# Kernel optimization log

Hardware: AMD Instinct MI355X
Metric: run time of the kernel (lower is better)

Reference implementation:

```python
import jax, jax.numpy as jnp
import numpy as np

IN_SIZE = 65536
HIDDEN = 128
D_STEPS = 64   # nd_actions[0]
N_ACT = 512    # nd_actions[1]


def setup_inputs() -> dict:
    key = jax.random.key(0)
    ks = jax.random.split(key, 7)
    s = 1.0 / np.sqrt(HIDDEN)  # torch LSTMCell/Linear init scale (uniform); use scaled normal
    return {
        "x": jax.random.normal(ks[0], (IN_SIZE,), jnp.float32),
        "w_ih": jax.random.normal(ks[1], (4 * HIDDEN, IN_SIZE), jnp.float32) * s,
        "w_hh": jax.random.normal(ks[2], (4 * HIDDEN, HIDDEN), jnp.float32) * s,
        "b_ih": jax.random.normal(ks[3], (4 * HIDDEN,), jnp.float32) * s,
        "b_hh": jax.random.normal(ks[4], (4 * HIDDEN,), jnp.float32) * s,
        "w_lin": jax.random.normal(ks[5], (N_ACT, HIDDEN), jnp.float32) * s,
        "b_lin": jax.random.normal(ks[6], (N_ACT,), jnp.float32) * s,
    }


def reference(x, w_ih, w_hh, b_ih, b_hh, w_lin, b_lin):
    # x is constant across the D steps, so its gate contribution is computed once.
    ihx = w_ih @ x + b_ih + b_hh  # (4H,)
    h0 = jnp.zeros((HIDDEN,), x.dtype)
    c0 = jnp.zeros((HIDDEN,), x.dtype)

    def step(carry, _):
        h, c = carry
        gates = ihx + w_hh @ h  # (4H,)
        i, f, g, o = jnp.split(gates, 4)  # torch LSTMCell gate order: i, f, g, o
        c = jax.nn.sigmoid(f) * c + jax.nn.sigmoid(i) * jnp.tanh(g)
        h = jax.nn.sigmoid(o) * jnp.tanh(c)
        logits = w_lin @ h + b_lin  # (N,)
        return (h, c), logits

    _, action_probs = jax.lax.scan(step, (h0, c0), None, length=D_STEPS)
    return action_probs  # (D, N)
```

## Files before the change

kernel.cpp:

```cpp
#include <hip/hip_runtime.h>
#include <hip/hip_bf16.h>

#define IN_SIZE 65536
#define HIDDEN 128
#define D_STEPS 64
#define N_ACT 512

typedef _Float16 half2_ __attribute__((ext_vector_type(2)));
typedef _Float16 half4_ __attribute__((ext_vector_type(4)));
typedef _Float16 half8_ __attribute__((ext_vector_type(8)));
typedef float f32x4 __attribute__((ext_vector_type(4)));

__device__ __forceinline__ float rcp_(float x) {
#if __has_builtin(__builtin_amdgcn_rcpf)
    return __builtin_amdgcn_rcpf(x);
#else
    return 1.f / x;
#endif
}
__device__ __forceinline__ float exp2_(float x) {
#if __has_builtin(__builtin_amdgcn_exp2f)
    return __builtin_amdgcn_exp2f(x);
#else
    return __exp2f(x);
#endif
}
#define L2E 1.44269504088896340736f

__global__ __launch_bounds__(256) void k_ihx(const float* __restrict__ w_ih,
                                             const float* __restrict__ x,
                                             float* __restrict__ partials) {
    int bid = blockIdx.x;
    int rp = bid >> 3;
    int ck = bid & 7;
    int t = threadIdx.x;
    int r0 = 2 * rp, r1 = 2 * rp + 1;
    const float4* xp = (const float4*)(x + ck * 8192);
    const float4* w0 = (const float4*)(w_ih + (size_t)r0 * IN_SIZE + ck * 8192);
    const float4* w1 = (const float4*)(w_ih + (size_t)r1 * IN_SIZE + ck * 8192);

    float4 xv[8];
#pragma unroll
    for (int i = 0; i < 8; ++i) xv[i] = xp[t + i * 256];

    float a0 = 0.f, a1 = 0.f;
#pragma unroll
    for (int i = 0; i < 8; ++i) {
        float4 w4 = w0[t + i * 256];
        a0 += w4.x * xv[i].x + w4.y * xv[i].y + w4.z * xv[i].z + w4.w * xv[i].w;
    }
#pragma unroll
    for (int i = 0; i < 8; ++i) {
        float4 w4 = w1[t + i * 256];
        a1 += w4.x * xv[i].x + w4.y * xv[i].y + w4.z * xv[i].z + w4.w * xv[i].w;
    }
#pragma unroll
    for (int off = 32; off; off >>= 1) {
        a0 += __shfl_down(a0, off, 64);
        a1 += __shfl_down(a1, off, 64);
    }
    __shared__ float s[8];
    if ((t & 63) == 0) { s[t >> 6] = a0; s[4 + (t >> 6)] = a1; }
    __syncthreads();
    if (t == 0) {
        partials[r0 * 8 + ck] = s[0] + s[1] + s[2] + s[3];
        partials[r1 * 8 + ck] = s[4] + s[5] + s[6] + s[7];
    }
}

__global__ __attribute__((amdgpu_flat_work_group_size(512, 512)))
__attribute__((amdgpu_waves_per_eu(2, 2)))
void k_rec_logits(
    const float* __restrict__ w_hh,
    const float* __restrict__ b_ih,
    const float* __restrict__ b_hh,
    const float* __restrict__ w_lin,
    const float* __restrict__ b_lin,
    const float* __restrict__ partials,
    float* __restrict__ out) {
    int t = threadIdx.x;
    int b = blockIdx.x;
    int w = t >> 6;
    int l = t & 63;
    int lg = l >> 4;
    int lm = l & 15;

    __shared__ _Float16 whh_s[4 * HIDDEN * HIDDEN];
    __shared__ half8_ h_v[2][16];
    __shared__ float h_keep[HIDDEN];
    __shared__ float ihx_s[4 * HIDDEN];

    {
        const float2* src = (const float2*)w_hh;
        half2_* dst = (half2_*)whh_s;
#pragma unroll 4
        for (int i = 0; i < 64; ++i) {
            float2 v = src[i * 512 + t];
            half2_ p = {(_Float16)v.x, (_Float16)v.y};
            dst[i * 512 + t] = p;
        }
    }
    {
        const float4* pp = (const float4*)(partials + t * 8);
        float4 p0 = pp[0], p1 = pp[1];
        ihx_s[t] = p0.x + p0.y + p0.z + p0.w + p1.x + p1.y + p1.z + p1.w +
                   b_ih[t] + b_hh[t];
    }
    if (t < 16) {
        half8_ z = {(_Float16)0.f, (_Float16)0.f, (_Float16)0.f, (_Float16)0.f,
                    (_Float16)0.f, (_Float16)0.f, (_Float16)0.f, (_Float16)0.f};
        h_v[0][t] = z;
    }
    __syncthreads();

    half8_ afrag[4][4];
#pragma unroll
    for (int G = 0; G < 4; ++G) {
#pragma unroll
        for (int kt = 0; kt < 4; ++kt) {
            afrag[G][kt] = *(const half8_*)&whh_s[(size_t)(G * HIDDEN + 16 * w + lm) * HIDDEN
                                                  + kt * 32 + lg * 8];
        }
    }
    f32x4 ihxv[4];
#pragma unroll
    for (int G = 0; G < 4; ++G)
        ihxv[G] = *(const f32x4*)&ihx_s[G * HIDDEN + 16 * w + lg * 4];

    asm volatile(""
        : "+v"(afrag[0][0]), "+v"(afrag[0][1]), "+v"(afrag[0][2]), "+v"(afrag[0][3]),
          "+v"(afrag[1][0]), "+v"(afrag[1][1]), "+v"(afrag[1][2]), "+v"(afrag[1][3]),
          "+v"(afrag[2][0]), "+v"(afrag[2][1]), "+v"(afrag[2][2]), "+v"(afrag[2][3]),
          "+v"(afrag[3][0]), "+v"(afrag[3][1]), "+v"(afrag[3][2]), "+v"(afrag[3][3]),
          "+v"(ihxv[0]), "+v"(ihxv[1]), "+v"(ihxv[2]), "+v"(ihxv[3]));

    int r2 = lm & 3;
    bool s1 = (r2 & 1) != 0, s2 = (r2 & 2) != 0;
    float c_own = 0.f;

    for (int d = 0; d < D_STEPS; ++d) {
        int rb = d & 1, wb = rb ^ 1;
        half8_ bf0 = h_v[rb][0 * 4 + lg];
        half8_ bf1 = h_v[rb][1 * 4 + lg];
        half8_ bf2 = h_v[rb][2 * 4 + lg];
        half8_ bf3 = h_v[rb][3 * 4 + lg];
        f32x4 ai_ = ihxv[0];
        f32x4 af_ = ihxv[1];
        f32x4 ag_ = ihxv[2];
        f32x4 ao_ = ihxv[3];
#define MFMA __builtin_amdgcn_mfma_f32_16x16x32_f16
        ai_ = MFMA(afrag[0][0], bf0, ai_, 0, 0, 0);
        af_ = MFMA(afrag[1][0], bf0, af_, 0, 0, 0);
        ag_ = MFMA(afrag[2][0], bf0, ag_, 0, 0, 0);
        ao_ = MFMA(afrag[3][0], bf0, ao_, 0, 0, 0);
        ai_ = MFMA(afrag[0][1], bf1, ai_, 0, 0, 0);
        af_ = MFMA(afrag[1][1], bf1, af_, 0, 0, 0);
        ag_ = MFMA(afrag[2][1], bf1, ag_, 0, 0, 0);
        ao_ = MFMA(afrag[3][1], bf1, ao_, 0, 0, 0);
        ai_ = MFMA(afrag[0][2], bf2, ai_, 0, 0, 0);
        af_ = MFMA(afrag[1][2], bf2, af_, 0, 0, 0);
        ag_ = MFMA(afrag[2][2], bf2, ag_, 0, 0, 0);
        ao_ = MFMA(afrag[3][2], bf2, ao_, 0, 0, 0);
        ai_ = MFMA(afrag[0][3], bf3, ai_, 0, 0, 0);
        af_ = MFMA(afrag[1][3], bf3, af_, 0, 0, 0);
        ag_ = MFMA(afrag[2][3], bf3, ag_, 0, 0, 0);
        ao_ = MFMA(afrag[3][3], bf3, ao_, 0, 0, 0);
#undef MFMA
        float gi = s2 ? (s1 ? ai_[3] : ai_[2]) : (s1 ? ai_[1] : ai_[0]);
        float gf = s2 ? (s1 ? af_[3] : af_[2]) : (s1 ? af_[1] : af_[0]);
        float gg = s2 ? (s1 ? ag_[3] : ag_[2]) : (s1 ? ag_[1] : ag_[0]);
        float go = s2 ? (s1 ? ao_[3] : ao_[2]) : (s1 ? ao_[1] : ao_[0]);
        float ig = rcp_(1.f + exp2_(-L2E * gi));
        float fg = rcp_(1.f + exp2_(-L2E * gf));
        float gt = 2.f * rcp_(1.f + exp2_(-2.f * L2E * gg)) - 1.f;
        float og = rcp_(1.f + exp2_(-L2E * go));
        c_own = fg * c_own + ig * gt;
        float th = 2.f * rcp_(1.f + exp2_(-2.f * L2E * c_own)) - 1.f;
        float h = og * th;
        if (lm < 4) {
            int cell = 16 * w + lg * 4 + r2;
            ((_Float16*)&h_v[wb][0])[cell] = (_Float16)h;
            if (d == b) h_keep[cell] = h;
        }
        __syncthreads();
    }

    {
        const float4* wl = (const float4*)(w_lin + (size_t)t * HIDDEN);
        float acc = b_lin[t];
#pragma unroll
        for (int k = 0; k < HIDDEN / 4; ++k) {
            float4 w4 = wl[k];
            acc += w4.x * h_keep[4 * k + 0] + w4.y * h_keep[4 * k + 1] +
                   w4.z * h_keep[4 * k + 2] + w4.w * h_keep[4 * k + 3];
        }
        out[b * N_ACT + t] = acc;
    }
}

extern "C" void kernel_launch(void* const* d_in, const int* in_sizes, int n_in,
                              void* d_out, int out_size, void* d_ws, size_t ws_size,
                              hipStream_t stream) {
    const float* x     = (const float*)d_in[0];
    const float* w_ih  = (const float*)d_in[1];
    const float* w_hh  = (const float*)d_in[2];
    const float* b_ih  = (const float*)d_in[3];
    const float* b_hh  = (const float*)d_in[4];
    const float* w_lin = (const float*)d_in[5];
    const float* b_lin = (const float*)d_in[6];
    float* out = (float*)d_out;

    float* partials = (float*)d_ws;

    k_ihx<<<2048, 256, 0, stream>>>(w_ih, x, partials);
    k_rec_logits<<<D_STEPS, 512, 0, stream>>>(w_hh, b_ih, b_hh, w_lin, b_lin,
                                              partials, out);
}
```

Baseline: 69.69 us.

## Halve recurrence block to 4 waves, each computing 32 hidden units

The recurrent kernel now runs 256 threads (4 waves) per block instead of 512. Each wave holds twice as many W_hh fragments in registers and issues 32 MFMAs per step covering 32 hidden cells. The intent is to make the per-step __syncthreads barrier cheaper with fewer waves, at the cost of longer MFMA chains per wave and higher register pressure. Setup and the final logits loop are split across two rows per thread to cover the same work.

```diff
diff --git a/kernel.cpp b/kernel.cpp
--- a/kernel.cpp
+++ b/kernel.cpp
@@ -7,7 +7,6 @@
 #define N_ACT 512
 
 typedef _Float16 half2_ __attribute__((ext_vector_type(2)));
-typedef _Float16 half4_ __attribute__((ext_vector_type(4)));
 typedef _Float16 half8_ __attribute__((ext_vector_type(8)));
 typedef float f32x4 __attribute__((ext_vector_type(4)));
 
@@ -68,8 +67,8 @@
     }
 }
 
-__global__ __attribute__((amdgpu_flat_work_group_size(512, 512)))
-__attribute__((amdgpu_waves_per_eu(2, 2)))
+__global__ __attribute__((amdgpu_flat_work_group_size(256, 256)))
+__attribute__((amdgpu_waves_per_eu(1, 1)))
 void k_rec_logits(
     const float* __restrict__ w_hh,
     const float* __restrict__ b_ih,
@@ -83,7 +82,7 @@
     int w = t >> 6;
     int l = t & 63;
     int lg = l >> 4;
-    int lm = l & 15;
+    int n  = l & 15;
 
     __shared__ _Float16 whh_s[4 * HIDDEN * HIDDEN];
     __shared__ half8_ h_v[2][16];
@@ -93,18 +92,20 @@
     {
         const float2* src = (const float2*)w_hh;
         half2_* dst = (half2_*)whh_s;
-#pragma unroll 4
-        for (int i = 0; i < 64; ++i) {
-            float2 v = src[i * 512 + t];
+#pragma unroll 8
+        for (int i = 0; i < 128; ++i) {
+            float2 v = src[i * 256 + t];
             half2_ p = {(_Float16)v.x, (_Float16)v.y};
-            dst[i * 512 + t] = p;
+            dst[i * 256 + t] = p;
         }
     }
-    {
-        const float4* pp = (const float4*)(partials + t * 8);
+#pragma unroll
+    for (int rr = 0; rr < 2; ++rr) {
+        int row = t + rr * 256;
+        const float4* pp = (const float4*)(partials + row * 8);
         float4 p0 = pp[0], p1 = pp[1];
-        ihx_s[t] = p0.x + p0.y + p0.z + p0.w + p1.x + p1.y + p1.z + p1.w +
-                   b_ih[t] + b_hh[t];
+        ihx_s[row] = p0.x + p0.y + p0.z + p0.w + p1.x + p1.y + p1.z + p1.w +
+                     b_ih[row] + b_hh[row];
     }
     if (t < 16) {
         half8_ z = {(_Float16)0.f, (_Float16)0.f, (_Float16)0.f, (_Float16)0.f,
@@ -113,29 +114,35 @@
     }
     __syncthreads();
 
-    half8_ afrag[4][4];
-#pragma unroll
-    for (int G = 0; G < 4; ++G) {
-#pragma unroll
-        for (int kt = 0; kt < 4; ++kt) {
-            afrag[G][kt] = *(const half8_*)&whh_s[(size_t)(G * HIDDEN + 16 * w + lm) * HIDDEN
-                                                  + kt * 32 + lg * 8];
-        }
-    }
-    f32x4 ihxv[4];
+    half8_ af[4][2][4];
 #pragma unroll
     for (int G = 0; G < 4; ++G)
-        ihxv[G] = *(const f32x4*)&ihx_s[G * HIDDEN + 16 * w + lg * 4];
-
-    asm volatile(""
-        : "+v"(afrag[0][0]), "+v"(afrag[0][1]), "+v"(afrag[0][2]), "+v"(afrag[0][3]),
-          "+v"(afrag[1][0]), "+v"(afrag[1][1]), "+v"(afrag[1][2]), "+v"(afrag[1][3]),
-          "+v"(afrag[2][0]), "+v"(afrag[2][1]), "+v"(afrag[2][2]), "+v"(afrag[2][3]),
-          "+v"(afrag[3][0]), "+v"(afrag[3][1]), "+v"(afrag[3][2]), "+v"(afrag[3][3]),
-          "+v"(ihxv[0]), "+v"(ihxv[1]), "+v"(ihxv[2]), "+v"(ihxv[3]));
-
-    int r2 = lm & 3;
-    bool s1 = (r2 & 1) != 0, s2 = (r2 & 2) != 0;
+#pragma unroll
+        for (int hh = 0; hh < 2; ++hh)
+#pragma unroll
+            for (int kt = 0; kt < 4; ++kt)
+                af[G][hh][kt] = *(const half8_*)&whh_s[
+                    (size_t)(G * HIDDEN + 32 * w + 16 * hh + n) * HIDDEN + kt * 32 + lg * 8];
+    f32x4 ihxv[4][2];
+#pragma unroll
+    for (int G = 0; G < 4; ++G)
+#pragma unroll
+        for (int hh = 0; hh < 2; ++hh)
+            ihxv[G][hh] = *(const f32x4*)&ihx_s[G * HIDDEN + 32 * w + 16 * hh + lg * 4];
+
+    asm volatile("" : "+v"(af[0][0][0]), "+v"(af[0][0][1]), "+v"(af[0][0][2]), "+v"(af[0][0][3]),
+                      "+v"(af[0][1][0]), "+v"(af[0][1][1]), "+v"(af[0][1][2]), "+v"(af[0][1][3]));
+    asm volatile("" : "+v"(af[1][0][0]), "+v"(af[1][0][1]), "+v"(af[1][0][2]), "+v"(af[1][0][3]),
+                      "+v"(af[1][1][0]), "+v"(af[1][1][1]), "+v"(af[1][1][2]), "+v"(af[1][1][3]));
+    asm volatile("" : "+v"(af[2][0][0]), "+v"(af[2][0][1]), "+v"(af[2][0][2]), "+v"(af[2][0][3]),
+                      "+v"(af[2][1][0]), "+v"(af[2][1][1]), "+v"(af[2][1][2]), "+v"(af[2][1][3]));
+    asm volatile("" : "+v"(af[3][0][0]), "+v"(af[3][0][1]), "+v"(af[3][0][2]), "+v"(af[3][0][3]),
+                      "+v"(af[3][1][0]), "+v"(af[3][1][1]), "+v"(af[3][1][2]), "+v"(af[3][1][3]));
+    asm volatile("" : "+v"(ihxv[0][0]), "+v"(ihxv[0][1]), "+v"(ihxv[1][0]), "+v"(ihxv[1][1]),
+                      "+v"(ihxv[2][0]), "+v"(ihxv[2][1]), "+v"(ihxv[3][0]), "+v"(ihxv[3][1]));
+
+    bool bh = (n & 4) != 0;
+    bool s1 = (n & 1) != 0, s2 = (n & 2) != 0;
     float c_own = 0.f;
 
     for (int d = 0; d < D_STEPS; ++d) {
@@ -144,32 +151,33 @@
         half8_ bf1 = h_v[rb][1 * 4 + lg];
         half8_ bf2 = h_v[rb][2 * 4 + lg];
         half8_ bf3 = h_v[rb][3 * 4 + lg];
-        f32x4 ai_ = ihxv[0];
-        f32x4 af_ = ihxv[1];
-        f32x4 ag_ = ihxv[2];
-        f32x4 ao_ = ihxv[3];
+        f32x4 a00 = ihxv[0][0], a01 = ihxv[0][1];
+        f32x4 a10 = ihxv[1][0], a11 = ihxv[1][1];
+        f32x4 a20 = ihxv[2][0], a21 = ihxv[2][1];
+        f32x4 a30 = ihxv[3][0], a31 = ihxv[3][1];
 #define MFMA __builtin_amdgcn_mfma_f32_16x16x32_f16
-        ai_ = MFMA(afrag[0][0], bf0, ai_, 0, 0, 0);
-        af_ = MFMA(afrag[1][0], bf0, af_, 0, 0, 0);
-        ag_ = MFMA(afrag[2][0], bf0, ag_, 0, 0, 0);
-        ao_ = MFMA(afrag[3][0], bf0, ao_, 0, 0, 0);
-        ai_ = MFMA(afrag[0][1], bf1, ai_, 0, 0, 0);
-        af_ = MFMA(afrag[1][1], bf1, af_, 0, 0, 0);
-        ag_ = MFMA(afrag[2][1], bf1, ag_, 0, 0, 0);
-        ao_ = MFMA(afrag[3][1], bf1, ao_, 0, 0, 0);
-        ai_ = MFMA(afrag[0][2], bf2, ai_, 0, 0, 0);
-        af_ = MFMA(afrag[1][2], bf2, af_, 0, 0, 0);
-        ag_ = MFMA(afrag[2][2], bf2, ag_, 0, 0, 0);
-        ao_ = MFMA(afrag[3][2], bf2, ao_, 0, 0, 0);
-        ai_ = MFMA(afrag[0][3], bf3, ai_, 0, 0, 0);
-        af_ = MFMA(afrag[1][3], bf3, af_, 0, 0, 0);
-        ag_ = MFMA(afrag[2][3], bf3, ag_, 0, 0, 0);
-        ao_ = MFMA(afrag[3][3], bf3, ao_, 0, 0, 0);
+#define KSTEP(kt, bf) \
+        a00 = MFMA(af[0][0][kt], bf, a00, 0, 0, 0); \
+        a01 = MFMA(af[0][1][kt], bf, a01, 0, 0, 0); \
+        a10 = MFMA(af[1][0][kt], bf, a10, 0, 0, 0); \
+        a11 = MFMA(af[1][1][kt], bf, a11, 0, 0, 0); \
+        a20 = MFMA(af[2][0][kt], bf, a20, 0, 0, 0); \
+        a21 = MFMA(af[2][1][kt], bf, a21, 0, 0, 0); \
+        a30 = MFMA(af[3][0][kt], bf, a30, 0, 0, 0); \
+        a31 = MFMA(af[3][1][kt], bf, a31, 0, 0, 0);
+        KSTEP(0, bf0)
+        KSTEP(1, bf1)
+        KSTEP(2, bf2)
+        KSTEP(3, bf3)
+#undef KSTEP
 #undef MFMA
-        float gi = s2 ? (s1 ? ai_[3] : ai_[2]) : (s1 ? ai_[1] : ai_[0]);
-        float gf = s2 ? (s1 ? af_[3] : af_[2]) : (s1 ? af_[1] : af_[0]);
-        float gg = s2 ? (s1 ? ag_[3] : ag_[2]) : (s1 ? ag_[1] : ag_[0]);
-        float go = s2 ? (s1 ? ao_[3] : ao_[2]) : (s1 ? ao_[1] : ao_[0]);
+#define PICK(v0, v1) (bh ? (s2 ? (s1 ? (v1)[3] : (v1)[2]) : (s1 ? (v1)[1] : (v1)[0])) \
+                         : (s2 ? (s1 ? (v0)[3] : (v0)[2]) : (s1 ? (v0)[1] : (v0)[0])))
+        float gi = PICK(a00, a01);
+        float gf = PICK(a10, a11);
+        float gg = PICK(a20, a21);
+        float go = PICK(a30, a31);
+#undef PICK
         float ig = rcp_(1.f + exp2_(-L2E * gi));
         float fg = rcp_(1.f + exp2_(-L2E * gf));
         float gt = 2.f * rcp_(1.f + exp2_(-2.f * L2E * gg)) - 1.f;
@@ -177,24 +185,26 @@
         c_own = fg * c_own + ig * gt;
         float th = 2.f * rcp_(1.f + exp2_(-2.f * L2E * c_own)) - 1.f;
         float h = og * th;
-        if (lm < 4) {
-            int cell = 16 * w + lg * 4 + r2;
+        if (n < 8) {
+            int cell = 32 * w + 16 * (n >> 2) + lg * 4 + (n & 3);
             ((_Float16*)&h_v[wb][0])[cell] = (_Float16)h;
             if (d == b) h_keep[cell] = h;
         }
         __syncthreads();
     }
 
-    {
-        const float4* wl = (const float4*)(w_lin + (size_t)t * HIDDEN);
-        float acc = b_lin[t];
+#pragma unroll
+    for (int rr = 0; rr < 2; ++rr) {
+        int row = t + rr * 256;
+        const float4* wl = (const float4*)(w_lin + (size_t)row * HIDDEN);
+        float acc = b_lin[row];
 #pragma unroll
         for (int k = 0; k < HIDDEN / 4; ++k) {
             float4 w4 = wl[k];
             acc += w4.x * h_keep[4 * k + 0] + w4.y * h_keep[4 * k + 1] +
                    w4.z * h_keep[4 * k + 2] + w4.w * h_keep[4 * k + 3];
         }
-        out[b * N_ACT + t] = acc;
+        out[b * N_ACT + row] = acc;
     }
 }
 
@@ -213,6 +223,6 @@
     float* partials = (float*)d_ws;
 
     k_ihx<<<2048, 256, 0, stream>>>(w_ih, x, partials);
-    k_rec_logits<<<D_STEPS, 512, 0, stream>>>(w_hh, b_ih, b_hh, w_lin, b_lin,
+    k_rec_logits<<<D_STEPS, 256, 0, stream>>>(w_hh, b_ih, b_hh, w_lin, b_lin,
                                               partials, out);
 }
```

Result: slower. 84.69 us (+21.5%).

## Pre-convert w_hh to fp16 in ihx kernel and split MFMA accumulation chains

Applied to the files above, without the earlier changes.

The fp32-to-fp16 conversion of w_hh moves into the first kernel, which writes an fp16 copy to workspace. The recurrent kernel then loads its MFMA A-fragments straight from global memory instead of staging 128KB through LDS, which drops a large LDS allocation and the prologue copy. The 16 dependent MFMAs per step are split into two independent accumulation chains that are summed at the end, shortening the dependency latency on the serial recurrence. The per-step h is also written unconditionally into a full h_all LDS array rather than under a branch, which trades 32KB of LDS for removing the d==b check.

```diff
diff --git a/kernel.cpp b/kernel.cpp
--- a/kernel.cpp
+++ b/kernel.cpp
@@ -29,11 +29,18 @@
 
 __global__ __launch_bounds__(256) void k_ihx(const float* __restrict__ w_ih,
                                              const float* __restrict__ x,
-                                             float* __restrict__ partials) {
+                                             const float* __restrict__ w_hh,
+                                             float* __restrict__ partials,
+                                             _Float16* __restrict__ whh16) {
     int bid = blockIdx.x;
+    int t = threadIdx.x;
+    if (t < 8) {
+        float4 v = ((const float4*)w_hh)[bid * 8 + t];
+        half4_ p = {(_Float16)v.x, (_Float16)v.y, (_Float16)v.z, (_Float16)v.w};
+        ((half4_*)whh16)[bid * 8 + t] = p;
+    }
     int rp = bid >> 3;
     int ck = bid & 7;
-    int t = threadIdx.x;
     int r0 = 2 * rp, r1 = 2 * rp + 1;
     const float4* xp = (const float4*)(x + ck * 8192);
     const float4* w0 = (const float4*)(w_ih + (size_t)r0 * IN_SIZE + ck * 8192);
@@ -71,7 +78,7 @@
 __global__ __attribute__((amdgpu_flat_work_group_size(512, 512)))
 __attribute__((amdgpu_waves_per_eu(2, 2)))
 void k_rec_logits(
-    const float* __restrict__ w_hh,
+    const _Float16* __restrict__ whh16,
     const float* __restrict__ b_ih,
     const float* __restrict__ b_hh,
     const float* __restrict__ w_lin,
@@ -85,21 +92,17 @@
     int lg = l >> 4;
     int lm = l & 15;
 
-    __shared__ _Float16 whh_s[4 * HIDDEN * HIDDEN];
     __shared__ half8_ h_v[2][16];
-    __shared__ float h_keep[HIDDEN];
+    __shared__ float h_all[D_STEPS][HIDDEN];
     __shared__ float ihx_s[4 * HIDDEN];
 
-    {
-        const float2* src = (const float2*)w_hh;
-        half2_* dst = (half2_*)whh_s;
-#pragma unroll 4
-        for (int i = 0; i < 64; ++i) {
-            float2 v = src[i * 512 + t];
-            half2_ p = {(_Float16)v.x, (_Float16)v.y};
-            dst[i * 512 + t] = p;
-        }
-    }
+    half8_ afrag[4][4];
+#pragma unroll
+    for (int G = 0; G < 4; ++G)
+#pragma unroll
+        for (int kt = 0; kt < 4; ++kt)
+            afrag[G][kt] = *(const half8_*)&whh16[(size_t)(G * HIDDEN + 16 * w + lm) * HIDDEN
+                                                  + kt * 32 + lg * 8];
     {
         const float4* pp = (const float4*)(partials + t * 8);
         float4 p0 = pp[0], p1 = pp[1];
@@ -113,15 +116,6 @@
     }
     __syncthreads();
 
-    half8_ afrag[4][4];
-#pragma unroll
-    for (int G = 0; G < 4; ++G) {
-#pragma unroll
-        for (int kt = 0; kt < 4; ++kt) {
-            afrag[G][kt] = *(const half8_*)&whh_s[(size_t)(G * HIDDEN + 16 * w + lm) * HIDDEN
-                                                  + kt * 32 + lg * 8];
-        }
-    }
     f32x4 ihxv[4];
 #pragma unroll
     for (int G = 0; G < 4; ++G)
@@ -137,6 +131,7 @@
     int r2 = lm & 3;
     bool s1 = (r2 & 1) != 0, s2 = (r2 & 2) != 0;
     float c_own = 0.f;
+    const f32x4 zr = {0.f, 0.f, 0.f, 0.f};
 
     for (int d = 0; d < D_STEPS; ++d) {
         int rb = d & 1, wb = rb ^ 1;
@@ -144,28 +139,28 @@
         half8_ bf1 = h_v[rb][1 * 4 + lg];
         half8_ bf2 = h_v[rb][2 * 4 + lg];
         half8_ bf3 = h_v[rb][3 * 4 + lg];
-        f32x4 ai_ = ihxv[0];
-        f32x4 af_ = ihxv[1];
-        f32x4 ag_ = ihxv[2];
-        f32x4 ao_ = ihxv[3];
 #define MFMA __builtin_amdgcn_mfma_f32_16x16x32_f16
-        ai_ = MFMA(afrag[0][0], bf0, ai_, 0, 0, 0);
-        af_ = MFMA(afrag[1][0], bf0, af_, 0, 0, 0);
-        ag_ = MFMA(afrag[2][0], bf0, ag_, 0, 0, 0);
-        ao_ = MFMA(afrag[3][0], bf0, ao_, 0, 0, 0);
-        ai_ = MFMA(afrag[0][1], bf1, ai_, 0, 0, 0);
-        af_ = MFMA(afrag[1][1], bf1, af_, 0, 0, 0);
-        ag_ = MFMA(afrag[2][1], bf1, ag_, 0, 0, 0);
-        ao_ = MFMA(afrag[3][1], bf1, ao_, 0, 0, 0);
-        ai_ = MFMA(afrag[0][2], bf2, ai_, 0, 0, 0);
-        af_ = MFMA(afrag[1][2], bf2, af_, 0, 0, 0);
-        ag_ = MFMA(afrag[2][2], bf2, ag_, 0, 0, 0);
-        ao_ = MFMA(afrag[3][2], bf2, ao_, 0, 0, 0);
-        ai_ = MFMA(afrag[0][3], bf3, ai_, 0, 0, 0);
-        af_ = MFMA(afrag[1][3], bf3, af_, 0, 0, 0);
-        ag_ = MFMA(afrag[2][3], bf3, ag_, 0, 0, 0);
-        ao_ = MFMA(afrag[3][3], bf3, ao_, 0, 0, 0);
+        f32x4 ai_a = MFMA(afrag[0][0], bf0, ihxv[0], 0, 0, 0);
+        f32x4 af_a = MFMA(afrag[1][0], bf0, ihxv[1], 0, 0, 0);
+        f32x4 ag_a = MFMA(afrag[2][0], bf0, ihxv[2], 0, 0, 0);
+        f32x4 ao_a = MFMA(afrag[3][0], bf0, ihxv[3], 0, 0, 0);
+        f32x4 ai_b = MFMA(afrag[0][1], bf1, zr, 0, 0, 0);
+        f32x4 af_b = MFMA(afrag[1][1], bf1, zr, 0, 0, 0);
+        f32x4 ag_b = MFMA(afrag[2][1], bf1, zr, 0, 0, 0);
+        f32x4 ao_b = MFMA(afrag[3][1], bf1, zr, 0, 0, 0);
+        ai_a = MFMA(afrag[0][2], bf2, ai_a, 0, 0, 0);
+        af_a = MFMA(afrag[1][2], bf2, af_a, 0, 0, 0);
+        ag_a = MFMA(afrag[2][2], bf2, ag_a, 0, 0, 0);
+        ao_a = MFMA(afrag[3][2], bf2, ao_a, 0, 0, 0);
+        ai_b = MFMA(afrag[0][3], bf3, ai_b, 0, 0, 0);
+        af_b = MFMA(afrag[1][3], bf3, af_b, 0, 0, 0);
+        ag_b = MFMA(afrag[2][3], bf3, ag_b, 0, 0, 0);
+        ao_b = MFMA(afrag[3][3], bf3, ao_b, 0, 0, 0);
 #undef MFMA
+        f32x4 ai_ = ai_a + ai_b;
+        f32x4 af_ = af_a + af_b;
+        f32x4 ag_ = ag_a + ag_b;
+        f32x4 ao_ = ao_a + ao_b;
         float gi = s2 ? (s1 ? ai_[3] : ai_[2]) : (s1 ? ai_[1] : ai_[0]);
         float gf = s2 ? (s1 ? af_[3] : af_[2]) : (s1 ? af_[1] : af_[0]);
         float gg = s2 ? (s1 ? ag_[3] : ag_[2]) : (s1 ? ag_[1] : ag_[0]);
@@ -180,19 +175,20 @@
         if (lm < 4) {
             int cell = 16 * w + lg * 4 + r2;
             ((_Float16*)&h_v[wb][0])[cell] = (_Float16)h;
-            if (d == b) h_keep[cell] = h;
+            h_all[d][cell] = h;
         }
         __syncthreads();
     }
 
     {
+        const float* hs = h_all[b];
         const float4* wl = (const float4*)(w_lin + (size_t)t * HIDDEN);
         float acc = b_lin[t];
 #pragma unroll
         for (int k = 0; k < HIDDEN / 4; ++k) {
             float4 w4 = wl[k];
-            acc += w4.x * h_keep[4 * k + 0] + w4.y * h_keep[4 * k + 1] +
-                   w4.z * h_keep[4 * k + 2] + w4.w * h_keep[4 * k + 3];
+            acc += w4.x * hs[4 * k + 0] + w4.y * hs[4 * k + 1] +
+                   w4.z * hs[4 * k + 2] + w4.w * hs[4 * k + 3];
         }
         out[b * N_ACT + t] = acc;
     }
@@ -210,9 +206,10 @@
     const float* b_lin = (const float*)d_in[6];
     float* out = (float*)d_out;
 
-    float* partials = (float*)d_ws;
-
-    k_ihx<<<2048, 256, 0, stream>>>(w_ih, x, partials);
-    k_rec_logits<<<D_STEPS, 512, 0, stream>>>(w_hh, b_ih, b_hh, w_lin, b_lin,
+    float* partials  = (float*)d_ws;
+    _Float16* whh16  = (_Float16*)((float*)d_ws + 4096);
+
+    k_ihx<<<2048, 256, 0, stream>>>(w_ih, x, w_hh, partials, whh16);
+    k_rec_logits<<<D_STEPS, 512, 0, stream>>>(whh16, b_ih, b_hh, w_lin, b_lin,
                                               partials, out);
 }
```

Measured after the change: 70.05 us. About the same (+0.5%).
